# Kernel optimization log

Hardware: AMD Instinct MI355X
Metric: run time of the kernel (lower is better)

The kernel has to match this reference:

```python
import math
import jax, jax.numpy as jnp
import numpy as np

N, C, H, W = 32, 128, 56, 56


def unfold3(x, axis, dil):
    """F.unfold with 3-tap kernel along `axis`, dilation `dil`, padding `dil`.
    Input (n,c,h,w) -> output (n,c,3,h,w); tap k takes offset (k-1)*dil."""
    pad_cfg = [(0, 0)] * 4
    pad_cfg[axis] = (dil, dil)
    xp = jnp.pad(x, pad_cfg)
    size = x.shape[axis]
    taps = [jax.lax.slice_in_dim(xp, k * dil, k * dil + size, axis=axis) for k in range(3)]
    return jnp.stack(taps, axis=2)


def setup_inputs() -> dict:
    key = jax.random.key(0)
    k0, k1, k2, k3, k4 = jax.random.split(key, 5)
    x = jax.random.normal(k0, (N, C, H, W), dtype=jnp.float32)
    # trunc_normal_(std=0.02) approximated by normal * 0.02
    p2 = jax.random.normal(k1, (1, 1, 3, 1, W), dtype=jnp.float32) * 0.02
    # 1x1 conv weight (out=C, in=3C), kaiming-ish scale
    p3 = jax.random.normal(k2, (C, 3 * C), dtype=jnp.float32) * (1.0 / math.sqrt(3 * C))
    p5 = jax.random.normal(k3, (1, 1, H, W), dtype=jnp.float32) * 0.02
    p10 = jax.random.normal(k4, (1, C, 3, H, W), dtype=jnp.float32) * 0.02
    return {"x": x, "p2": p2, "p3": p3, "p5": p5, "p10": p10}


def reference(x, p2, p3, p5, p10):
    n, c, h, w = x.shape
    # t_1: vertical 3-tap unfold, dilation 2 -> (n,c,3,h,w)
    t1 = unfold3(x, axis=2, dil=2)
    t2 = p2 * t1                                              # (n,c,3,h,w)
    # t_3: 1x1 conv over the c*3 channel view
    t3 = jnp.einsum('nkhw,ck->nchw', t1.reshape(n, c * 3, h, w), p3)
    # t_4: horizontal 3-tap unfold, dilation 1
    t4 = unfold3(t3, axis=3, dil=1)                           # (n,c,3,h,w)
    t5 = p5 * t3                                              # (n,c,h,w)
    # t_7/t_8: horizontal 3-tap unfold of x, dilation 2, softmax over taps
    t7 = unfold3(x, axis=3, dil=2)
    t8 = jax.nn.softmax(t7, axis=2)                           # (n,c,3,h,w)
    # t_9: bmm over spatial dim -> (n,c,c*3)
    t9 = jnp.einsum('ncx,ndx->ncd', x.reshape(n, c, h * w),
                    t4.reshape(n, c * 3, h * w)) / math.sqrt(h * w)
    t10 = p10 * t8                                            # (n,c,3,h,w)
    # t_11: memory-reinterpreting view: (n,1,c,h,w) - (n,3,c,h,w) -> back to (n,c,3,h,w)
    t11 = (t5[:, None] - t2.reshape(n, 3, c, h, w)).reshape(n, c, 3, h, w)
    t12 = t11 - t10                                           # (n,c,3,h,w)
    # t_13: bmm over c*3 -> (n,c,h*w)
    t13 = jnp.einsum('ncd,ndx->ncx', t9,
                     t12.reshape(n, c * 3, h * w)) / math.sqrt(c * 3)
    return t13.reshape(n, c, h, w)
```

## Files before the change

### kernel.cpp

```cpp
#include <hip/hip_runtime.h>
#include <stdint.h>

#define NB 32
#define C_ 128
#define H_ 56
#define W_ 56
#define HW 3136
#define KD 384

typedef __attribute__((ext_vector_type(8))) short bf16x8;
typedef __attribute__((ext_vector_type(4))) float f32x4;

__device__ inline uint16_t f2bf(float f) {
    uint32_t u = __float_as_uint(f);
    return (uint16_t)((u + 0x7FFFu + ((u >> 16) & 1u)) >> 16);
}
__device__ inline float bf2f(uint16_t b) {
    return __uint_as_float(((uint32_t)b) << 16);
}

__global__ __launch_bounds__(256) void p1_xtp(const float* __restrict__ x,
                                              uint16_t* __restrict__ xtp) {
    __shared__ uint16_t lt[56][136];
    const int h = blockIdx.x, n = blockIdx.y, tid = threadIdx.x;
    const int c = tid >> 1, wh = tid & 1;
    const float* xr = &x[(((size_t)n * C_ + c) * H_ + h) * W_ + wh * 28];
#pragma unroll
    for (int q = 0; q < 7; ++q) {
        float4 v = *(const float4*)&xr[q * 4];
        int wb = wh * 28 + q * 4;
        lt[wb + 0][c] = f2bf(v.x);
        lt[wb + 1][c] = f2bf(v.y);
        lt[wb + 2][c] = f2bf(v.z);
        lt[wb + 3][c] = f2bf(v.w);
    }
    __syncthreads();
    const int w = tid >> 2, qc = tid & 3;
    uint16_t* dst = &xtp[((((size_t)n * H_ + h) * 64 + w)) * C_ + qc * 32];
    if (w < 56) {
        const uint32_t* s = (const uint32_t*)&lt[w][qc * 32];
        uint4 a = *(const uint4*)(s);
        uint4 b = *(const uint4*)(s + 4);
        uint4 c4 = *(const uint4*)(s + 8);
        uint4 d4 = *(const uint4*)(s + 12);
        *(uint4*)dst = a;
        *(uint4*)(dst + 8) = b;
        *(uint4*)(dst + 16) = c4;
        *(uint4*)(dst + 24) = d4;
    } else {
        uint4 z = {0, 0, 0, 0};
        *(uint4*)dst = z;
        *(uint4*)(dst + 8) = z;
        *(uint4*)(dst + 16) = z;
        *(uint4*)(dst + 24) = z;
    }
}

__global__ __launch_bounds__(256) void p2_ap(const float* __restrict__ p3,
                                             uint16_t* __restrict__ ap) {
    int i = blockIdx.x * 256 + threadIdx.x;
    int c = i / KD, dp = i - c * KD;
    int tap = dp >> 7, c2 = dp & 127;
    ap[i] = f2bf(p3[c * KD + 3 * c2 + tap]);
}

__global__ __launch_bounds__(256) void k1(const uint16_t* __restrict__ xtp,
                                          const uint16_t* __restrict__ ap,
                                          uint16_t* __restrict__ t3b) {
    __shared__ uint16_t smem[3 * 64 * 128];
    const int h = blockIdx.x, n = blockIdx.y, tid = threadIdx.x;
    const int lane = tid & 63, wid = tid >> 6;
    const int wm = wid >> 1, wn = wid & 1;

    for (int t = tid; t < 3072; t += 256) {
        int tap = t >> 10, r = t & 1023, w = r >> 4, qp = r & 15;
        int q = qp ^ (w & 7);
        int hh = h + 2 * (tap - 1);
        uint4 v = {0, 0, 0, 0};
        if ((unsigned)hh < (unsigned)H_)
            v = *(const uint4*)&xtp[((((size_t)n * H_ + hh) * 64 + w)) * C_ + q * 8];
        *(uint4*)&smem[tap * 8192 + w * 128 + qp * 8] = v;
    }
    __syncthreads();

    f32x4 acc[4][2] = {};
    for (int ks = 0; ks < 12; ++ks) {
        int tap = ks >> 2, kk = ks & 3;
        bf16x8 a[4], b[2];
#pragma unroll
        for (int m = 0; m < 4; ++m) {
            int c = wm * 64 + m * 16 + (lane & 15);
            a[m] = *(const bf16x8*)&ap[c * KD + ks * 32 + (lane >> 4) * 8];
        }
#pragma unroll
        for (int nt = 0; nt < 2; ++nt) {
            int w = wn * 32 + nt * 16 + (lane & 15);
            int q = kk * 4 + (lane >> 4);
            b[nt] = *(const bf16x8*)&smem[tap * 8192 + w * 128 + (q ^ (w & 7)) * 8];
        }
#pragma unroll
        for (int m = 0; m < 4; ++m)
#pragma unroll
            for (int nt = 0; nt < 2; ++nt)
                acc[m][nt] = __builtin_amdgcn_mfma_f32_16x16x32_bf16(a[m], b[nt], acc[m][nt], 0, 0, 0);
    }
    __syncthreads();

    uint16_t* lrow = smem;
#pragma unroll
    for (int m = 0; m < 4; ++m)
#pragma unroll
        for (int nt = 0; nt < 2; ++nt)
#pragma unroll
            for (int r = 0; r < 4; ++r) {
                int c = wm * 64 + m * 16 + (lane >> 4) * 4 + r;
                int w = wn * 32 + nt * 16 + (lane & 15);
                lrow[c * 72 + w] = f2bf(acc[m][nt][r]);
            }
    __syncthreads();

    const uint32_t* lrowd = (const uint32_t*)smem;
    for (int t = tid; t < 1024; t += 256) {
        int c = t >> 3, ch = t & 7;
        int m0 = c * 36 + ch * 4;
        uint4 o = make_uint4(lrowd[m0], lrowd[m0 + 1], lrowd[m0 + 2], lrowd[m0 + 3]);
        *(uint4*)&t3b[(((size_t)n * C_ + c) * H_ + h) * 64 + ch * 8] = o;
    }
}

__global__ __launch_bounds__(512) void k2(const float* __restrict__ x,
                                          const uint16_t* __restrict__ t3b,
                                          float* __restrict__ part) {
    __shared__ uint16_t xs[128 * 64];
    __shared__ uint16_t ts[128 * 64];
    const int bx = blockIdx.x;
    const int hc = bx / 3, tap = bx - hc * 3;
    const int n = blockIdx.y;
    const int tid = threadIdx.x, lane = tid & 63, wid = tid >> 6;
    const int wm = wid >> 2, wn = wid & 3;

    f32x4 acc[4][2] = {};
    for (int hr = 0; hr < 8; ++hr) {
        const int h = hc * 8 + hr;
        __syncthreads();
        for (int t = tid; t < 1024; t += 512) {
            int c = t >> 3, qp = t & 7, q = qp ^ (c & 7);
            uint4 v = {0, 0, 0, 0};
            if (q < 7) {
                const float* s = &x[(((size_t)n * C_ + c) * H_ + h) * W_ + q * 8];
                float4 f0 = *(const float4*)s, f1 = *(const float4*)(s + 4);
                v.x = (uint32_t)f2bf(f0.x) | ((uint32_t)f2bf(f0.y) << 16);
                v.y = (uint32_t)f2bf(f0.z) | ((uint32_t)f2bf(f0.w) << 16);
                v.z = (uint32_t)f2bf(f1.x) | ((uint32_t)f2bf(f1.y) << 16);
                v.w = (uint32_t)f2bf(f1.z) | ((uint32_t)f2bf(f1.w) << 16);
            }
            *(uint4*)&xs[c * 64 + qp * 8] = v;
        }
        for (int t = tid; t < 1024; t += 512) {
            int c2 = t >> 3, qp = t & 7, q = qp ^ (c2 & 7);
            const uint16_t* row = &t3b[(((size_t)n * C_ + c2) * H_ + h) * 64];
            uint4 v = *(const uint4*)&row[q * 8];
            uint4 o;
            if (tap == 1) {
                o = v;
            } else if (tap == 2) {
                uint32_t nx = (q < 7) ? *(const uint32_t*)&row[q * 8 + 8] : 0u;
                o.x = (v.y << 16) | (v.x >> 16);
                o.y = (v.z << 16) | (v.y >> 16);
                o.z = (v.w << 16) | (v.z >> 16);
                o.w = (nx << 16)  | (v.w >> 16);
            } else {
                uint32_t pv = (q > 0) ? *(const uint32_t*)&row[q * 8 - 2] : 0u;
                o.x = (v.x << 16) | (pv >> 16);
                o.y = (v.y << 16) | (v.x >> 16);
                o.z = (v.z << 16) | (v.y >> 16);
                o.w = (v.w << 16) | (v.z >> 16);
            }
            *(uint4*)&ts[c2 * 64 + qp * 8] = o;
        }
        __syncthreads();
#pragma unroll
        for (int ks = 0; ks < 2; ++ks) {
            bf16x8 a[4], b[2];
#pragma unroll
            for (int m = 0; m < 4; ++m) {
                int c = wm * 64 + m * 16 + (lane & 15);
                int q = ks * 4 + (lane >> 4);
                a[m] = *(const bf16x8*)&xs[c * 64 + (q ^ (c & 7)) * 8];
            }
#pragma unroll
            for (int nt = 0; nt < 2; ++nt) {
                int c2 = wn * 32 + nt * 16 + (lane & 15);
                int q = ks * 4 + (lane >> 4);
                b[nt] = *(const bf16x8*)&ts[c2 * 64 + (q ^ (c2 & 7)) * 8];
            }
#pragma unroll
            for (int m = 0; m < 4; ++m)
#pragma unroll
                for (int nt = 0; nt < 2; ++nt)
                    acc[m][nt] = __builtin_amdgcn_mfma_f32_16x16x32_bf16(a[m], b[nt], acc[m][nt], 0, 0, 0);
        }
    }
#pragma unroll
    for (int m = 0; m < 4; ++m)
#pragma unroll
        for (int nt = 0; nt < 2; ++nt)
#pragma unroll
            for (int r = 0; r < 4; ++r) {
                int c = wm * 64 + m * 16 + (lane >> 4) * 4 + r;
                int col = wn * 32 + nt * 16 + (lane & 15);
                part[((((size_t)bx * NB + n) * C_ + c) << 7) + col] = acc[m][nt][r];
            }
}

__global__ __launch_bounds__(256) void kr(const float* __restrict__ part,
                                          uint16_t* __restrict__ acat) {
    int idx = blockIdx.x * 256 + threadIdx.x;
    int fl = idx * 4;
    int nc = fl / KD, dp = fl - nc * KD;
    int tap = dp >> 7, c2 = dp & 127;
    float4 s = make_float4(0.f, 0.f, 0.f, 0.f);
#pragma unroll
    for (int hc = 0; hc < 7; ++hc) {
        const float4 v = *(const float4*)&part[((((size_t)(hc * 3 + tap)) * NB * C_ + nc) << 7) + c2];
        s.x += v.x; s.y += v.y; s.z += v.z; s.w += v.w;
    }
    const float sc = 1.f / 56.f;
    uint2 o;
    o.x = (uint32_t)f2bf(s.x * sc) | ((uint32_t)f2bf(s.y * sc) << 16);
    o.y = (uint32_t)f2bf(s.z * sc) | ((uint32_t)f2bf(s.w * sc) << 16);
    *(uint2*)&acat[(size_t)nc * 512 + dp] = o;
}

__global__ __launch_bounds__(256) void ka2(uint16_t* __restrict__ acat) {
    int t = blockIdx.x * 256 + threadIdx.x;
    int nc = t >> 3, m0 = (t & 7) * 16;
    uint16_t* row = &acat[(size_t)nc * 512];
#pragma unroll
    for (int mi = 0; mi < 16; ++mi) {
        int m = m0 + mi;
        float s = 0.f;
#pragma unroll
        for (int r = 0; r < 3; ++r) {
            int d = m + 128 * r;
            int q3 = d / 3;
            int dp = (d - q3 * 3) * 128 + q3;
            s += bf2f(row[dp]);
        }
        row[384 + m] = f2bf(s);
    }
}

__global__ __launch_bounds__(256) void kt(const float* __restrict__ p10,
                                          uint16_t* __restrict__ p10t) {
    const int h = blockIdx.x, tid = threadIdx.x;
    for (int idx = tid; idx < 3072; idx += 256) {
        int w = idx & 63, ch = idx >> 6;
        int dp0 = ch * 8;
        uint32_t pk[4];
#pragma unroll
        for (int j = 0; j < 8; ++j) {
            int dp = dp0 + j;
            int tap = dp >> 7, c2 = dp & 127;
            int dor = 3 * c2 + tap;
            float v = (w < W_) ? p10[(size_t)dor * HW + h * W_ + w] : 0.f;
            uint16_t bb = f2bf(v);
            if (j & 1) pk[j >> 1] |= ((uint32_t)bb) << 16;
            else       pk[j >> 1] = bb;
        }
        *(uint4*)&p10t[((size_t)h * 64 + w) * KD + dp0] = *(const uint4*)pk;
    }
}

__global__ __launch_bounds__(256, 4) void k3(const uint16_t* __restrict__ xtp,
                                             const uint16_t* __restrict__ t3b,
                                             const uint16_t* __restrict__ acat,
                                             const uint16_t* __restrict__ p10t,
                                             const float* __restrict__ p2,
                                             const float* __restrict__ p5,
                                             float* __restrict__ out) {
    __shared__ uint16_t tsm[32 * 512];
    const int bx = blockIdx.x, n = blockIdx.y, tid = threadIdx.x;
    const int h = bx >> 1, wbase = (bx & 1) << 5;
    const int lane = tid & 63, wid = tid >> 6;

    {
        const int w = tid & 31, seg = tid >> 5;
        const int wg = wbase + w;
        const int wsw = w & 7;
        float p2v[3];
#pragma unroll
        for (int tap = 0; tap < 3; ++tap)
            p2v[tap] = (wg < W_) ? p2[tap * W_ + wg] : 0.f;
        const size_t xrow = ((size_t)n * H_ + h) * 64;
        const int wgm2 = (wg >= 2) ? wg - 2 : 0;
        const int wgp2 = (wg + 2 < 64) ? wg + 2 : 63;

#pragma unroll
        for (int s = 0; s < 2; ++s) {
            const int c2b = (seg + s * 8) * 8;
            bf16x8 xh_v = *(const bf16x8*)&xtp[(xrow + wg) * C_ + c2b];
            bf16x8 xm_v = *(const bf16x8*)&xtp[(xrow + wgm2) * C_ + c2b];
            bf16x8 xp_v = *(const bf16x8*)&xtp[(xrow + wgp2) * C_ + c2b];
            float sm[3][8];
#pragma unroll
            for (int j = 0; j < 8; ++j) {
                float a1 = bf2f((uint16_t)xh_v[j]);
                float a0 = (wg >= 2) ? bf2f((uint16_t)xm_v[j]) : 0.f;
                float a2 = bf2f((uint16_t)xp_v[j]);
                float mx = fmaxf(a0, fmaxf(a1, a2));
                float e0 = __expf(a0 - mx), e1 = __expf(a1 - mx), e2 = __expf(a2 - mx);
                float rs = 1.f / (e0 + e1 + e2);
                sm[0][j] = e0 * rs; sm[1][j] = e1 * rs; sm[2][j] = e2 * rs;
            }
#pragma unroll
            for (int tap = 0; tap < 3; ++tap) {
                bf16x8 xhh;
                float p2e;
                if (tap == 1) { xhh = xh_v; p2e = p2v[1]; }
                else {
                    const int hh = h + 2 * (tap - 1);
                    const bool hok = (unsigned)hh < (unsigned)H_;
                    const int hhc = hok ? hh : h;
                    xhh = *(const bf16x8*)&xtp[(((size_t)n * H_ + hhc) * 64 + wg) * C_ + c2b];
                    p2e = hok ? p2v[tap] : 0.f;
                }
                bf16x8 pv = *(const bf16x8*)&p10t[((size_t)h * 64 + wg) * KD + tap * 128 + c2b];
                uint32_t pk[4];
#pragma unroll
                for (int j = 0; j < 8; ++j) {
                    float val = -(p2e * bf2f((uint16_t)xhh[j]) + bf2f((uint16_t)pv[j]) * sm[tap][j]);
                    uint16_t bb = f2bf(val);
                    if (j & 1) pk[j >> 1] |= ((uint32_t)bb) << 16;
                    else       pk[j >> 1] = bb;
                }
                int q = (tap * 128 + c2b) >> 3;
                *(uint4*)&tsm[w * 512 + ((q ^ wsw) << 3)] = *(const uint4*)pk;
            }
        }
    }

    {
        const int c2f = tid >> 1;
        const int whl = (tid & 1) << 4;
        const uint16_t* t3r = &t3b[(((size_t)n * C_ + c2f) * H_ + h) * 64 + wbase + whl];
        const int qf = 48 + (c2f >> 3);
        const int cf7 = c2f & 7;
#pragma unroll
        for (int g = 0; g < 2; ++g) {
            bf16x8 tv = *(const bf16x8*)&t3r[g * 8];
#pragma unroll
            for (int j = 0; j < 8; ++j) {
                int wl = whl + g * 8 + j;
                int wwg = wbase + wl;
                float p5v = (wwg < W_) ? p5[h * W_ + wwg] : 0.f;
                tsm[wl * 512 + ((qf ^ (wl & 7)) << 3) + cf7] = f2bf(p5v * bf2f((uint16_t)tv[j]));
            }
        }
    }
    __syncthreads();

    const int wm = wid;
    f32x4 acc[2][2] = {};
    for (int ks = 0; ks < 16; ++ks) {
        bf16x8 a[2], b[2];
#pragma unroll
        for (int m = 0; m < 2; ++m) {
            int c = wm * 32 + m * 16 + (lane & 15);
            a[m] = *(const bf16x8*)&acat[((size_t)n * C_ + c) * 512 + ks * 32 + (lane >> 4) * 8];
        }
#pragma unroll
        for (int nt = 0; nt < 2; ++nt) {
            int wl = nt * 16 + (lane & 15);
            int q = ks * 4 + (lane >> 4);
            b[nt] = *(const bf16x8*)&tsm[wl * 512 + ((q ^ (wl & 7)) << 3)];
        }
#pragma unroll
        for (int m = 0; m < 2; ++m)
#pragma unroll
            for (int nt = 0; nt < 2; ++nt)
                acc[m][nt] = __builtin_amdgcn_mfma_f32_16x16x32_bf16(a[m], b[nt], acc[m][nt], 0, 0, 0);
    }

    const float s = 0.05103103630798287f;
#pragma unroll
    for (int m = 0; m < 2; ++m)
#pragma unroll
        for (int nt = 0; nt < 2; ++nt) {
            int wwg = wbase + nt * 16 + (lane & 15);
            if (wwg < W_) {
                int c = wm * 32 + m * 16 + (lane >> 4) * 4;
                float* dst = &out[(((size_t)n * C_ + c) * H_ + h) * W_ + wwg];
#pragma unroll
                for (int r = 0; r < 4; ++r) dst[(size_t)r * HW] = acc[m][nt][r] * s;
            }
        }
}

extern "C" void kernel_launch(void* const* d_in, const int* in_sizes, int n_in,
                              void* d_out, int out_size, void* d_ws, size_t ws_size,
                              hipStream_t stream) {
    const float* x   = (const float*)d_in[0];
    const float* p2  = (const float*)d_in[1];
    const float* p3  = (const float*)d_in[2];
    const float* p5  = (const float*)d_in[3];
    const float* p10 = (const float*)d_in[4];
    float* out = (float*)d_out;

    uint8_t* w8 = (uint8_t*)d_ws;
    uint16_t* t3b  = (uint16_t*)(w8);
    uint16_t* ap   = (uint16_t*)(w8 + 29360128);
    uint16_t* xtp  = (uint16_t*)(w8 + 29458432);
    float*    part = (float*)   (w8 + 58818560);
    uint16_t* p10t = (uint16_t*)(w8 + 58818560);
    uint16_t* acat = (uint16_t*)(w8 + 102858752);

    p1_xtp<<<dim3(H_, NB), 256, 0, stream>>>(x, xtp);
    p2_ap<<<dim3(192), 256, 0, stream>>>(p3, ap);
    k1<<<dim3(H_, NB), 256, 0, stream>>>(xtp, ap, t3b);
    k2<<<dim3(21, NB), 512, 0, stream>>>(x, t3b, part);
    kr<<<dim3(1536), 256, 0, stream>>>(part, acat);
    ka2<<<dim3(128), 256, 0, stream>>>(acat);
    kt<<<dim3(H_), 256, 0, stream>>>(p10, p10t);
    k3<<<dim3(112, NB), 256, 0, stream>>>(xtp, t3b, acat, p10t, p2, p5, out);
}
```

Measured before the change: 249.1 us.

## Build MFMA B operand in registers in k3, dropping shared-memory staging

The k3 kernel now builds each MFMA B fragment directly in registers from the elementwise softmax/p2/p10 and p5*t3 terms, rather than writing a 32x512 tile to LDS, syncing, and reading it back. Each block now covers a full row h (all 64 w columns, one per wave's 16-lane group) and computes all 128 output channels per wave, so the grid halves. This removes LDS traffic and the barrier. In exchange each wave reloads the full A matrix (acat) from global memory/cache, and the t3 loads become strided scalar reads.

```diff
diff --git a/kernel.cpp b/kernel.cpp
--- a/kernel.cpp
+++ b/kernel.cpp
@@ -279,122 +279,97 @@
                                              const float* __restrict__ p2,
                                              const float* __restrict__ p5,
                                              float* __restrict__ out) {
-    __shared__ uint16_t tsm[32 * 512];
-    const int bx = blockIdx.x, n = blockIdx.y, tid = threadIdx.x;
-    const int h = bx >> 1, wbase = (bx & 1) << 5;
+    const int h = blockIdx.x, n = blockIdx.y, tid = threadIdx.x;
     const int lane = tid & 63, wid = tid >> 6;
-
-    {
-        const int w = tid & 31, seg = tid >> 5;
-        const int wg = wbase + w;
-        const int wsw = w & 7;
-        float p2v[3];
-#pragma unroll
-        for (int tap = 0; tap < 3; ++tap)
-            p2v[tap] = (wg < W_) ? p2[tap * W_ + wg] : 0.f;
-        const size_t xrow = ((size_t)n * H_ + h) * 64;
-        const int wgm2 = (wg >= 2) ? wg - 2 : 0;
-        const int wgp2 = (wg + 2 < 64) ? wg + 2 : 63;
-
-#pragma unroll
-        for (int s = 0; s < 2; ++s) {
-            const int c2b = (seg + s * 8) * 8;
-            bf16x8 xh_v = *(const bf16x8*)&xtp[(xrow + wg) * C_ + c2b];
-            bf16x8 xm_v = *(const bf16x8*)&xtp[(xrow + wgm2) * C_ + c2b];
-            bf16x8 xp_v = *(const bf16x8*)&xtp[(xrow + wgp2) * C_ + c2b];
-            float sm[3][8];
+    const int c15 = lane & 15, kq = lane >> 4;
+    const int wg = wid * 16 + c15;
+
+    float p2v[3];
+#pragma unroll
+    for (int tap = 0; tap < 3; ++tap)
+        p2v[tap] = (wg < W_) ? p2[tap * W_ + wg] : 0.f;
+    const float p5v = (wg < W_) ? p5[h * W_ + wg] : 0.f;
+
+    const size_t xrow = ((size_t)n * H_ + h) * 64;
+    const int wgm2 = (wg >= 2) ? wg - 2 : 0;
+    const int wgp2 = (wg + 2 < 64) ? wg + 2 : 63;
+    const uint16_t* acN = acat + (size_t)n * C_ * 512;
+    const uint16_t* pt = &p10t[((size_t)h * 64 + wg) * KD];
+
+    f32x4 acc[8] = {};
+
+#pragma unroll
+    for (int ksub = 0; ksub < 4; ++ksub) {
+        const int c2b = ksub * 32 + kq * 8;
+        bf16x8 xh_v = *(const bf16x8*)&xtp[(xrow + wg) * C_ + c2b];
+        bf16x8 xm_v = *(const bf16x8*)&xtp[(xrow + wgm2) * C_ + c2b];
+        bf16x8 xp_v = *(const bf16x8*)&xtp[(xrow + wgp2) * C_ + c2b];
+        float sm[3][8];
+#pragma unroll
+        for (int j = 0; j < 8; ++j) {
+            float a1 = bf2f((uint16_t)xh_v[j]);
+            float a0 = (wg >= 2) ? bf2f((uint16_t)xm_v[j]) : 0.f;
+            float a2 = bf2f((uint16_t)xp_v[j]);
+            float mx = fmaxf(a0, fmaxf(a1, a2));
+            float e0 = __expf(a0 - mx), e1 = __expf(a1 - mx), e2 = __expf(a2 - mx);
+            float rs = 1.f / (e0 + e1 + e2);
+            sm[0][j] = e0 * rs; sm[1][j] = e1 * rs; sm[2][j] = e2 * rs;
+        }
+#pragma unroll
+        for (int tap = 0; tap < 3; ++tap) {
+            const int k0 = tap * 128 + c2b;
+            bf16x8 xhh;
+            float p2e;
+            if (tap == 1) { xhh = xh_v; p2e = p2v[1]; }
+            else {
+                const int hh = h + 2 * (tap - 1);
+                const bool hok = (unsigned)hh < (unsigned)H_;
+                const int hhc = hok ? hh : h;
+                xhh = *(const bf16x8*)&xtp[(((size_t)n * H_ + hhc) * 64 + wg) * C_ + c2b];
+                p2e = hok ? p2v[tap] : 0.f;
+            }
+            bf16x8 pv = *(const bf16x8*)&pt[k0];
+            bf16x8 b;
 #pragma unroll
             for (int j = 0; j < 8; ++j) {
-                float a1 = bf2f((uint16_t)xh_v[j]);
-                float a0 = (wg >= 2) ? bf2f((uint16_t)xm_v[j]) : 0.f;
-                float a2 = bf2f((uint16_t)xp_v[j]);
-                float mx = fmaxf(a0, fmaxf(a1, a2));
-                float e0 = __expf(a0 - mx), e1 = __expf(a1 - mx), e2 = __expf(a2 - mx);
-                float rs = 1.f / (e0 + e1 + e2);
-                sm[0][j] = e0 * rs; sm[1][j] = e1 * rs; sm[2][j] = e2 * rs;
-            }
-#pragma unroll
-            for (int tap = 0; tap < 3; ++tap) {
-                bf16x8 xhh;
-                float p2e;
-                if (tap == 1) { xhh = xh_v; p2e = p2v[1]; }
-                else {
-                    const int hh = h + 2 * (tap - 1);
-                    const bool hok = (unsigned)hh < (unsigned)H_;
-                    const int hhc = hok ? hh : h;
-                    xhh = *(const bf16x8*)&xtp[(((size_t)n * H_ + hhc) * 64 + wg) * C_ + c2b];
-                    p2e = hok ? p2v[tap] : 0.f;
-                }
-                bf16x8 pv = *(const bf16x8*)&p10t[((size_t)h * 64 + wg) * KD + tap * 128 + c2b];
-                uint32_t pk[4];
-#pragma unroll
-                for (int j = 0; j < 8; ++j) {
-                    float val = -(p2e * bf2f((uint16_t)xhh[j]) + bf2f((uint16_t)pv[j]) * sm[tap][j]);
-                    uint16_t bb = f2bf(val);
-                    if (j & 1) pk[j >> 1] |= ((uint32_t)bb) << 16;
-                    else       pk[j >> 1] = bb;
-                }
-                int q = (tap * 128 + c2b) >> 3;
-                *(uint4*)&tsm[w * 512 + ((q ^ wsw) << 3)] = *(const uint4*)pk;
-            }
-        }
-    }
-
-    {
-        const int c2f = tid >> 1;
-        const int whl = (tid & 1) << 4;
-        const uint16_t* t3r = &t3b[(((size_t)n * C_ + c2f) * H_ + h) * 64 + wbase + whl];
-        const int qf = 48 + (c2f >> 3);
-        const int cf7 = c2f & 7;
-#pragma unroll
-        for (int g = 0; g < 2; ++g) {
-            bf16x8 tv = *(const bf16x8*)&t3r[g * 8];
-#pragma unroll
-            for (int j = 0; j < 8; ++j) {
-                int wl = whl + g * 8 + j;
-                int wwg = wbase + wl;
-                float p5v = (wwg < W_) ? p5[h * W_ + wwg] : 0.f;
-                tsm[wl * 512 + ((qf ^ (wl & 7)) << 3) + cf7] = f2bf(p5v * bf2f((uint16_t)tv[j]));
-            }
-        }
-    }
-    __syncthreads();
-
-    const int wm = wid;
-    f32x4 acc[2][2] = {};
-    for (int ks = 0; ks < 16; ++ks) {
-        bf16x8 a[2], b[2];
-#pragma unroll
-        for (int m = 0; m < 2; ++m) {
-            int c = wm * 32 + m * 16 + (lane & 15);
-            a[m] = *(const bf16x8*)&acat[((size_t)n * C_ + c) * 512 + ks * 32 + (lane >> 4) * 8];
-        }
-#pragma unroll
-        for (int nt = 0; nt < 2; ++nt) {
-            int wl = nt * 16 + (lane & 15);
-            int q = ks * 4 + (lane >> 4);
-            b[nt] = *(const bf16x8*)&tsm[wl * 512 + ((q ^ (wl & 7)) << 3)];
-        }
-#pragma unroll
-        for (int m = 0; m < 2; ++m)
-#pragma unroll
-            for (int nt = 0; nt < 2; ++nt)
-                acc[m][nt] = __builtin_amdgcn_mfma_f32_16x16x32_bf16(a[m], b[nt], acc[m][nt], 0, 0, 0);
+                float val = -(p2e * bf2f((uint16_t)xhh[j]) + bf2f((uint16_t)pv[j]) * sm[tap][j]);
+                b[j] = (short)f2bf(val);
+            }
+#pragma unroll
+            for (int m = 0; m < 8; ++m) {
+                bf16x8 a = *(const bf16x8*)&acN[(size_t)(m * 16 + c15) * 512 + k0];
+                acc[m] = __builtin_amdgcn_mfma_f32_16x16x32_bf16(a, b, acc[m], 0, 0, 0);
+            }
+        }
+    }
+
+#pragma unroll
+    for (int ksub = 0; ksub < 4; ++ksub) {
+        const int c2b = ksub * 32 + kq * 8;
+        const int k0 = 384 + c2b;
+        bf16x8 b;
+#pragma unroll
+        for (int j = 0; j < 8; ++j) {
+            float t3v = bf2f(t3b[(((size_t)n * C_ + c2b + j) * H_ + h) * 64 + wg]);
+            b[j] = (short)f2bf(p5v * t3v);
+        }
+#pragma unroll
+        for (int m = 0; m < 8; ++m) {
+            bf16x8 a = *(const bf16x8*)&acN[(size_t)(m * 16 + c15) * 512 + k0];
+            acc[m] = __builtin_amdgcn_mfma_f32_16x16x32_bf16(a, b, acc[m], 0, 0, 0);
+        }
     }
 
     const float s = 0.05103103630798287f;
-#pragma unroll
-    for (int m = 0; m < 2; ++m)
-#pragma unroll
-        for (int nt = 0; nt < 2; ++nt) {
-            int wwg = wbase + nt * 16 + (lane & 15);
-            if (wwg < W_) {
-                int c = wm * 32 + m * 16 + (lane >> 4) * 4;
-                float* dst = &out[(((size_t)n * C_ + c) * H_ + h) * W_ + wwg];
-#pragma unroll
-                for (int r = 0; r < 4; ++r) dst[(size_t)r * HW] = acc[m][nt][r] * s;
-            }
-        }
+    if (wg < W_) {
+#pragma unroll
+        for (int m = 0; m < 8; ++m) {
+            int c = m * 16 + kq * 4;
+            float* dst = &out[(((size_t)n * C_ + c) * H_ + h) * W_ + wg];
+#pragma unroll
+            for (int r = 0; r < 4; ++r) dst[(size_t)r * HW] = acc[m][r] * s;
+        }
+    }
 }
 
 extern "C" void kernel_launch(void* const* d_in, const int* in_sizes, int n_in,
@@ -422,5 +397,5 @@
     kr<<<dim3(1536), 256, 0, stream>>>(part, acat);
     ka2<<<dim3(128), 256, 0, stream>>>(acat);
     kt<<<dim3(H_), 256, 0, stream>>>(p10, p10t);
-    k3<<<dim3(112, NB), 256, 0, stream>>>(xtp, t3b, acat, p10t, p2, p5, out);
-}
+    k3<<<dim3(H_, NB), 256, 0, stream>>>(xtp, t3b, acat, p10t, p2, p5, out);
+}
```

New measurement: 289.3 us. +16.1%, slower.
